# Performance work log

Hardware: AMD Instinct MI355X
Metric: run time of the kernel (lower is better)

Reference implementation:

```python
import jax, jax.numpy as jnp
import numpy as np

BATCH = 16384
N_MODES = 4096  # grid length == retained Fourier modes


def setup_inputs() -> dict:
    key = jax.random.key(0)
    k1, k2, k3 = jax.random.split(key, 3)
    inputs = jax.random.normal(k1, (BATCH, N_MODES), dtype=jnp.float32)
    # he_normal-style init for fourier weights, normal for linear weights
    fourier_weights = jax.random.normal(k2, (N_MODES,), dtype=jnp.float32) * np.sqrt(2.0 / N_MODES).astype(np.float32)
    linear_weights = jax.random.normal(k3, (N_MODES,), dtype=jnp.float32)
    return {"inputs": inputs, "fourier_weights": fourier_weights, "linear_weights": linear_weights}


def reference(inputs, fourier_weights, linear_weights):
    n_modes = fourier_weights.shape[0]
    # FFT along last axis (tf.signal.fft semantics), truncate to n_modes
    xf = jnp.fft.fft(inputs.astype(jnp.complex64), axis=-1)[:, :n_modes]
    # complex elementwise multiply by real weights cast to complex
    xf = xf * fourier_weights.astype(jnp.complex64)
    # inverse FFT over the truncated spectrum, take real part
    x = jnp.real(jnp.fft.ifft(xf, axis=-1)).astype(jnp.float32)
    # spectral branch scaled by linear weights + linear skip branch
    x = x * linear_weights
    z = inputs * linear_weights
    return jax.nn.relu(x + z)
```

## Files before the change

kernel.cpp:

```cpp
#include <hip/hip_runtime.h>
#include <math.h>

#define FFT_N   4096
#define THREADS 256
#define PADN    (FFT_N + (FFT_N >> 5))

__global__ void setup_g_kernel(const float* __restrict__ fw, float* __restrict__ gperm) {
    int p = blockIdx.x * blockDim.x + threadIdx.x;
    if (p >= FFT_N) return;
    unsigned k = ((p & 15u) << 8) | (p & 0xF0u) | ((unsigned)p >> 8);
    float wk  = fw[k];
    float wnk = fw[(FFT_N - k) & (FFT_N - 1)];
    gperm[p] = (0.5f * (wk + wnk) + 1.0f) * (1.0f / (float)FFT_N);
}

template<int DIR>
__device__ __forceinline__ void dft16(float xr[16], float xi[16]) {
    const float C1 = 0.9238795325112867f;
    const float S1 = 0.3826834323650898f;
    const float H  = 0.7071067811865476f;
    const float TCt[10] = {1.f, C1, H, S1, 0.f, -S1, -H, -C1, -1.f, -C1};
    const float TSt[10] = {0.f, S1, H, C1, 1.f,  C1, H,  S1,  0.f, -S1};
    float tr[16], ti[16];
    #pragma unroll
    for (int m0 = 0; m0 < 4; ++m0) {
        float ar = xr[m0+ 0], ai = xi[m0+ 0];
        float br = xr[m0+ 4], bi = xi[m0+ 4];
        float cr = xr[m0+ 8], ci = xi[m0+ 8];
        float dr = xr[m0+12], di = xi[m0+12];
        float t0r = ar+cr, t0i = ai+ci;
        float t1r = ar-cr, t1i = ai-ci;
        float t2r = br+dr, t2i = bi+di;
        float t3r = br-dr, t3i = bi-di;
        float A0r = t0r+t2r, A0i = t0i+t2i;
        float A2r = t0r-t2r, A2i = t0i-t2i;
        float A1r, A1i, A3r, A3i;
        if (DIR > 0) { A1r = t1r + t3i; A1i = t1i - t3r; A3r = t1r - t3i; A3i = t1i + t3r; }
        else         { A1r = t1r - t3i; A1i = t1i + t3r; A3r = t1r + t3i; A3i = t1i - t3r; }
        tr[0*4+m0] = A0r; ti[0*4+m0] = A0i;
        {
            float c = TCt[m0], s = (DIR > 0) ? -TSt[m0] : TSt[m0];
            float vr = A1r*c - A1i*s, vi = A1r*s + A1i*c;
            tr[1*4+m0] = vr; ti[1*4+m0] = vi;
        }
        {
            float c = TCt[2*m0], s = (DIR > 0) ? -TSt[2*m0] : TSt[2*m0];
            float vr = A2r*c - A2i*s, vi = A2r*s + A2i*c;
            tr[2*4+m0] = vr; ti[2*4+m0] = vi;
        }
        {
            float c = TCt[3*m0], s = (DIR > 0) ? -TSt[3*m0] : TSt[3*m0];
            float vr = A3r*c - A3i*s, vi = A3r*s + A3i*c;
            tr[3*4+m0] = vr; ti[3*4+m0] = vi;
        }
    }
    #pragma unroll
    for (int k0 = 0; k0 < 4; ++k0) {
        float ar = tr[k0*4+0], ai = ti[k0*4+0];
        float br = tr[k0*4+1], bi = ti[k0*4+1];
        float cr = tr[k0*4+2], ci = ti[k0*4+2];
        float dr = tr[k0*4+3], di = ti[k0*4+3];
        float t0r = ar+cr, t0i = ai+ci;
        float t1r = ar-cr, t1i = ai-ci;
        float t2r = br+dr, t2i = bi+di;
        float t3r = br-dr, t3i = bi-di;
        xr[k0+ 0] = t0r+t2r; xi[k0+ 0] = t0i+t2i;
        xr[k0+ 8] = t0r-t2r; xi[k0+ 8] = t0i-t2i;
        if (DIR > 0) {
            xr[k0+ 4] = t1r + t3i; xi[k0+ 4] = t1i - t3r;
            xr[k0+12] = t1r - t3i; xi[k0+12] = t1i + t3r;
        } else {
            xr[k0+ 4] = t1r - t3i; xi[k0+ 4] = t1i + t3r;
            xr[k0+12] = t1r + t3i; xi[k0+12] = t1i - t3r;
        }
    }
}

__device__ __forceinline__ void twiddle_apply(float xr[16], float xi[16], float ang1) {
    float s1, c1;
    __sincosf(ang1, &s1, &c1);
    float wc = c1, ws = s1;
    #pragma unroll
    for (int k = 1; k < 16; ++k) {
        float tv = xr[k];
        xr[k] = tv*wc - xi[k]*ws;
        xi[k] = tv*ws + xi[k]*wc;
        if (k < 15) { float nc = wc*c1 - ws*s1; ws = wc*s1 + ws*c1; wc = nc; }
    }
}

__global__ __launch_bounds__(THREADS, 4) void fourier_fft_kernel(
    const float* __restrict__ in, const float* __restrict__ gperm,
    const float* __restrict__ lw, float* __restrict__ out)
{
    __shared__ float re[PADN];
    __shared__ float im[PADN];
    const int t = threadIdx.x;
    const long long pair = blockIdx.x;
    const float* r0 = in + pair * (2LL * FFT_N);
    const float* r1 = r0 + FFT_N;

    const float CFA = -6.28318530717958647692f / 4096.0f;
    const float CFB = -6.28318530717958647692f / 256.0f;

    float xr[16], xi[16];

    #pragma unroll
    for (int k = 0; k < 16; ++k) {
        xr[k] = r0[t + 256*k];
        xi[k] = r1[t + 256*k];
    }

    dft16<1>(xr, xi);
    twiddle_apply(xr, xi, CFA * (float)t);
    #pragma unroll
    for (int k = 0; k < 16; ++k) { int s = t + 256*k; s += s>>5; re[s] = xr[k]; im[s] = xi[k]; }
    __syncthreads();

    const int jb = t & 15;
    const int baseB = (t >> 4)*256 + jb;
    #pragma unroll
    for (int k = 0; k < 16; ++k) { int s = baseB + 16*k; s += s>>5; xr[k] = re[s]; xi[k] = im[s]; }
    dft16<1>(xr, xi);
    twiddle_apply(xr, xi, CFB * (float)jb);
    #pragma unroll
    for (int k = 0; k < 16; ++k) { int s = baseB + 16*k; s += s>>5; re[s] = xr[k]; im[s] = xi[k]; }
    __syncthreads();

    #pragma unroll
    for (int k = 0; k < 16; ++k) { int s = 16*t + k; s += s>>5; xr[k] = re[s]; xi[k] = im[s]; }
    dft16<1>(xr, xi);
    {
        const float4* gp = (const float4*)(gperm + 16*t);
        #pragma unroll
        for (int q = 0; q < 4; ++q) {
            float4 g = gp[q];
            xr[4*q+0] *= g.x; xi[4*q+0] *= g.x;
            xr[4*q+1] *= g.y; xi[4*q+1] *= g.y;
            xr[4*q+2] *= g.z; xi[4*q+2] *= g.z;
            xr[4*q+3] *= g.w; xi[4*q+3] *= g.w;
        }
    }
    dft16<-1>(xr, xi);
    #pragma unroll
    for (int k = 0; k < 16; ++k) { int s = 16*t + k; s += s>>5; re[s] = xr[k]; im[s] = xi[k]; }
    __syncthreads();

    #pragma unroll
    for (int k = 0; k < 16; ++k) { int s = baseB + 16*k; s += s>>5; xr[k] = re[s]; xi[k] = im[s]; }
    twiddle_apply(xr, xi, -CFB * (float)jb);
    dft16<-1>(xr, xi);
    #pragma unroll
    for (int k = 0; k < 16; ++k) { int s = baseB + 16*k; s += s>>5; re[s] = xr[k]; im[s] = xi[k]; }
    __syncthreads();

    #pragma unroll
    for (int k = 0; k < 16; ++k) { int s = t + 256*k; s += s>>5; xr[k] = re[s]; xi[k] = im[s]; }
    twiddle_apply(xr, xi, -CFA * (float)t);
    dft16<-1>(xr, xi);

    float* o0 = out + pair * (2LL * FFT_N);
    #pragma unroll
    for (int k = 0; k < 16; ++k) {
        int i = t + 256*k;
        float l = lw[i];
        o0[i]         = fmaxf(xr[k]*l, 0.0f);
        o0[FFT_N + i] = fmaxf(xi[k]*l, 0.0f);
    }
}

extern "C" void kernel_launch(void* const* d_in, const int* in_sizes, int n_in,
                              void* d_out, int out_size, void* d_ws, size_t ws_size,
                              hipStream_t stream) {
    const float* inputs = (const float*)d_in[0];
    const float* fw     = (const float*)d_in[1];
    const float* lw     = (const float*)d_in[2];
    float* out   = (float*)d_out;
    float* gperm = (float*)d_ws;

    hipLaunchKernelGGL(setup_g_kernel, dim3(FFT_N / THREADS), dim3(THREADS), 0, stream,
                       fw, gperm);

    const int pairs = in_sizes[0] / (2 * FFT_N);
    hipLaunchKernelGGL(fourier_fft_kernel, dim3(pairs), dim3(THREADS), 0, stream,
                       inputs, gperm, lw, out);
}
```

Baseline: 119.8 us.

## Switch FFT from radix-16 three-pass to radix-8 four-pass with XOR-swizzled LDS

Rewrites the 4096-point forward/inverse FFT pair from three radix-16 passes with 256 threads into four radix-8 passes with 512 threads per block. This roughly halves per-thread register use so more waves can be resident, which should hide global and LDS latency better. Bank conflicts are now avoided with an XOR swizzle instead of padded shared arrays, and the gain-vector permutation is updated to the new digit-reversal order. In exchange there are more LDS round trips and barriers per row pair.

New measurement: 124.5 us. +4.0%, slower.

```diff
diff --git a/kernel.cpp b/kernel.cpp
--- a/kernel.cpp
+++ b/kernel.cpp
@@ -2,167 +2,165 @@
 #include <math.h>
 
 #define FFT_N   4096
-#define THREADS 256
-#define PADN    (FFT_N + (FFT_N >> 5))
+#define THREADS 512
+
+__device__ __forceinline__ int swz(int i) {
+    return i ^ ((i >> 5) & 31) ^ (((i >> 6) & 7) << 2);
+}
 
 __global__ void setup_g_kernel(const float* __restrict__ fw, float* __restrict__ gperm) {
     int p = blockIdx.x * blockDim.x + threadIdx.x;
     if (p >= FFT_N) return;
-    unsigned k = ((p & 15u) << 8) | (p & 0xF0u) | ((unsigned)p >> 8);
+    unsigned k = ((p & 7u) << 9) | (((p >> 3) & 7u) << 6) | (((p >> 6) & 7u) << 3) | ((p >> 9) & 7u);
     float wk  = fw[k];
     float wnk = fw[(FFT_N - k) & (FFT_N - 1)];
     gperm[p] = (0.5f * (wk + wnk) + 1.0f) * (1.0f / (float)FFT_N);
 }
 
 template<int DIR>
-__device__ __forceinline__ void dft16(float xr[16], float xi[16]) {
-    const float C1 = 0.9238795325112867f;
-    const float S1 = 0.3826834323650898f;
-    const float H  = 0.7071067811865476f;
-    const float TCt[10] = {1.f, C1, H, S1, 0.f, -S1, -H, -C1, -1.f, -C1};
-    const float TSt[10] = {0.f, S1, H, C1, 1.f,  C1, H,  S1,  0.f, -S1};
-    float tr[16], ti[16];
-    #pragma unroll
-    for (int m0 = 0; m0 < 4; ++m0) {
-        float ar = xr[m0+ 0], ai = xi[m0+ 0];
-        float br = xr[m0+ 4], bi = xi[m0+ 4];
-        float cr = xr[m0+ 8], ci = xi[m0+ 8];
-        float dr = xr[m0+12], di = xi[m0+12];
-        float t0r = ar+cr, t0i = ai+ci;
-        float t1r = ar-cr, t1i = ai-ci;
-        float t2r = br+dr, t2i = bi+di;
-        float t3r = br-dr, t3i = bi-di;
-        float A0r = t0r+t2r, A0i = t0i+t2i;
-        float A2r = t0r-t2r, A2i = t0i-t2i;
-        float A1r, A1i, A3r, A3i;
-        if (DIR > 0) { A1r = t1r + t3i; A1i = t1i - t3r; A3r = t1r - t3i; A3i = t1i + t3r; }
-        else         { A1r = t1r - t3i; A1i = t1i + t3r; A3r = t1r + t3i; A3i = t1i - t3r; }
-        tr[0*4+m0] = A0r; ti[0*4+m0] = A0i;
-        {
-            float c = TCt[m0], s = (DIR > 0) ? -TSt[m0] : TSt[m0];
-            float vr = A1r*c - A1i*s, vi = A1r*s + A1i*c;
-            tr[1*4+m0] = vr; ti[1*4+m0] = vi;
-        }
-        {
-            float c = TCt[2*m0], s = (DIR > 0) ? -TSt[2*m0] : TSt[2*m0];
-            float vr = A2r*c - A2i*s, vi = A2r*s + A2i*c;
-            tr[2*4+m0] = vr; ti[2*4+m0] = vi;
-        }
-        {
-            float c = TCt[3*m0], s = (DIR > 0) ? -TSt[3*m0] : TSt[3*m0];
-            float vr = A3r*c - A3i*s, vi = A3r*s + A3i*c;
-            tr[3*4+m0] = vr; ti[3*4+m0] = vi;
-        }
+__device__ __forceinline__ void dft8(float xr[8], float xi[8]) {
+    const float H = 0.7071067811865476f;
+    float u0r = xr[0]+xr[4], u0i = xi[0]+xi[4];
+    float u1r = xr[1]+xr[5], u1i = xi[1]+xi[5];
+    float u2r = xr[2]+xr[6], u2i = xi[2]+xi[6];
+    float u3r = xr[3]+xr[7], u3i = xi[3]+xi[7];
+    float v0r = xr[0]-xr[4], v0i = xi[0]-xi[4];
+    float v1r = xr[1]-xr[5], v1i = xi[1]-xi[5];
+    float v2r = xr[2]-xr[6], v2i = xi[2]-xi[6];
+    float v3r = xr[3]-xr[7], v3i = xi[3]-xi[7];
+    {
+        float r = v1r, m = v1i;
+        if (DIR > 0) { v1r = H*(r + m); v1i = H*(m - r); }
+        else         { v1r = H*(r - m); v1i = H*(m + r); }
     }
-    #pragma unroll
-    for (int k0 = 0; k0 < 4; ++k0) {
-        float ar = tr[k0*4+0], ai = ti[k0*4+0];
-        float br = tr[k0*4+1], bi = ti[k0*4+1];
-        float cr = tr[k0*4+2], ci = ti[k0*4+2];
-        float dr = tr[k0*4+3], di = ti[k0*4+3];
-        float t0r = ar+cr, t0i = ai+ci;
-        float t1r = ar-cr, t1i = ai-ci;
-        float t2r = br+dr, t2i = bi+di;
-        float t3r = br-dr, t3i = bi-di;
-        xr[k0+ 0] = t0r+t2r; xi[k0+ 0] = t0i+t2i;
-        xr[k0+ 8] = t0r-t2r; xi[k0+ 8] = t0i-t2i;
-        if (DIR > 0) {
-            xr[k0+ 4] = t1r + t3i; xi[k0+ 4] = t1i - t3r;
-            xr[k0+12] = t1r - t3i; xi[k0+12] = t1i + t3r;
-        } else {
-            xr[k0+ 4] = t1r - t3i; xi[k0+ 4] = t1i + t3r;
-            xr[k0+12] = t1r + t3i; xi[k0+12] = t1i - t3r;
-        }
+    {
+        float r = v2r, m = v2i;
+        if (DIR > 0) { v2r = m;  v2i = -r; }
+        else         { v2r = -m; v2i = r;  }
+    }
+    {
+        float r = v3r, m = v3i;
+        if (DIR > 0) { v3r = H*(m - r);  v3i = -H*(m + r); }
+        else         { v3r = -H*(m + r); v3i = H*(r - m);  }
+    }
+    {
+        float t0r=u0r+u2r, t0i=u0i+u2i, t1r=u0r-u2r, t1i=u0i-u2i;
+        float t2r=u1r+u3r, t2i=u1i+u3i, t3r=u1r-u3r, t3i=u1i-u3i;
+        xr[0]=t0r+t2r; xi[0]=t0i+t2i;
+        xr[4]=t0r-t2r; xi[4]=t0i-t2i;
+        if (DIR>0) { xr[2]=t1r+t3i; xi[2]=t1i-t3r; xr[6]=t1r-t3i; xi[6]=t1i+t3r; }
+        else       { xr[2]=t1r-t3i; xi[2]=t1i+t3r; xr[6]=t1r+t3i; xi[6]=t1i-t3r; }
+    }
+    {
+        float t0r=v0r+v2r, t0i=v0i+v2i, t1r=v0r-v2r, t1i=v0i-v2i;
+        float t2r=v1r+v3r, t2i=v1i+v3i, t3r=v1r-v3r, t3i=v1i-v3i;
+        xr[1]=t0r+t2r; xi[1]=t0i+t2i;
+        xr[5]=t0r-t2r; xi[5]=t0i-t2i;
+        if (DIR>0) { xr[3]=t1r+t3i; xi[3]=t1i-t3r; xr[7]=t1r-t3i; xi[7]=t1i+t3r; }
+        else       { xr[3]=t1r-t3i; xi[3]=t1i+t3r; xr[7]=t1r+t3i; xi[7]=t1i-t3r; }
     }
 }
 
-__device__ __forceinline__ void twiddle_apply(float xr[16], float xi[16], float ang1) {
-    float s1, c1;
-    __sincosf(ang1, &s1, &c1);
+__device__ __forceinline__ void twiddle8(float xr[8], float xi[8], float ang) {
+    float s1, c1; __sincosf(ang, &s1, &c1);
     float wc = c1, ws = s1;
     #pragma unroll
-    for (int k = 1; k < 16; ++k) {
+    for (int k = 1; k < 8; ++k) {
         float tv = xr[k];
         xr[k] = tv*wc - xi[k]*ws;
         xi[k] = tv*ws + xi[k]*wc;
-        if (k < 15) { float nc = wc*c1 - ws*s1; ws = wc*s1 + ws*c1; wc = nc; }
+        if (k < 7) { float nc = wc*c1 - ws*s1; ws = wc*s1 + ws*c1; wc = nc; }
     }
 }
 
-__global__ __launch_bounds__(THREADS, 4) void fourier_fft_kernel(
+__global__ __launch_bounds__(THREADS, 6) void fourier_fft_kernel(
     const float* __restrict__ in, const float* __restrict__ gperm,
     const float* __restrict__ lw, float* __restrict__ out)
 {
-    __shared__ float re[PADN];
-    __shared__ float im[PADN];
+    __shared__ float re[FFT_N];
+    __shared__ float im[FFT_N];
     const int t = threadIdx.x;
     const long long pair = blockIdx.x;
     const float* r0 = in + pair * (2LL * FFT_N);
     const float* r1 = r0 + FFT_N;
 
     const float CFA = -6.28318530717958647692f / 4096.0f;
-    const float CFB = -6.28318530717958647692f / 256.0f;
+    const float CFB = -6.28318530717958647692f / 512.0f;
+    const float CFC = -6.28318530717958647692f / 64.0f;
 
-    float xr[16], xi[16];
+    float xr[8], xi[8];
 
     #pragma unroll
-    for (int k = 0; k < 16; ++k) {
-        xr[k] = r0[t + 256*k];
-        xi[k] = r1[t + 256*k];
+    for (int k = 0; k < 8; ++k) {
+        xr[k] = r0[t + 512*k];
+        xi[k] = r1[t + 512*k];
     }
 
-    dft16<1>(xr, xi);
-    twiddle_apply(xr, xi, CFA * (float)t);
+    dft8<1>(xr, xi);
+    twiddle8(xr, xi, CFA * (float)t);
     #pragma unroll
-    for (int k = 0; k < 16; ++k) { int s = t + 256*k; s += s>>5; re[s] = xr[k]; im[s] = xi[k]; }
+    for (int k = 0; k < 8; ++k) { int s = swz(t + 512*k); re[s] = xr[k]; im[s] = xi[k]; }
     __syncthreads();
 
-    const int jb = t & 15;
-    const int baseB = (t >> 4)*256 + jb;
+    const int baseB = ((t >> 6) << 9) + (t & 63);
     #pragma unroll
-    for (int k = 0; k < 16; ++k) { int s = baseB + 16*k; s += s>>5; xr[k] = re[s]; xi[k] = im[s]; }
-    dft16<1>(xr, xi);
-    twiddle_apply(xr, xi, CFB * (float)jb);
+    for (int k = 0; k < 8; ++k) { int s = swz(baseB + 64*k); xr[k] = re[s]; xi[k] = im[s]; }
+    dft8<1>(xr, xi);
+    twiddle8(xr, xi, CFB * (float)(t & 63));
     #pragma unroll
-    for (int k = 0; k < 16; ++k) { int s = baseB + 16*k; s += s>>5; re[s] = xr[k]; im[s] = xi[k]; }
+    for (int k = 0; k < 8; ++k) { int s = swz(baseB + 64*k); re[s] = xr[k]; im[s] = xi[k]; }
+    __syncthreads();
+
+    const int baseC = ((t >> 3) << 6) + (t & 7);
+    #pragma unroll
+    for (int k = 0; k < 8; ++k) { int s = swz(baseC + 8*k); xr[k] = re[s]; xi[k] = im[s]; }
+    dft8<1>(xr, xi);
+    twiddle8(xr, xi, CFC * (float)(t & 7));
+    #pragma unroll
+    for (int k = 0; k < 8; ++k) { int s = swz(baseC + 8*k); re[s] = xr[k]; im[s] = xi[k]; }
     __syncthreads();
 
     #pragma unroll
-    for (int k = 0; k < 16; ++k) { int s = 16*t + k; s += s>>5; xr[k] = re[s]; xi[k] = im[s]; }
-    dft16<1>(xr, xi);
+    for (int k = 0; k < 8; ++k) { int s = swz(8*t + k); xr[k] = re[s]; xi[k] = im[s]; }
+    dft8<1>(xr, xi);
     {
-        const float4* gp = (const float4*)(gperm + 16*t);
-        #pragma unroll
-        for (int q = 0; q < 4; ++q) {
-            float4 g = gp[q];
-            xr[4*q+0] *= g.x; xi[4*q+0] *= g.x;
-            xr[4*q+1] *= g.y; xi[4*q+1] *= g.y;
-            xr[4*q+2] *= g.z; xi[4*q+2] *= g.z;
-            xr[4*q+3] *= g.w; xi[4*q+3] *= g.w;
-        }
+        const float4* gp = (const float4*)(gperm + 8*t);
+        float4 g0 = gp[0], g1 = gp[1];
+        xr[0] *= g0.x; xi[0] *= g0.x;  xr[1] *= g0.y; xi[1] *= g0.y;
+        xr[2] *= g0.z; xi[2] *= g0.z;  xr[3] *= g0.w; xi[3] *= g0.w;
+        xr[4] *= g1.x; xi[4] *= g1.x;  xr[5] *= g1.y; xi[5] *= g1.y;
+        xr[6] *= g1.z; xi[6] *= g1.z;  xr[7] *= g1.w; xi[7] *= g1.w;
     }
-    dft16<-1>(xr, xi);
+    dft8<-1>(xr, xi);
     #pragma unroll
-    for (int k = 0; k < 16; ++k) { int s = 16*t + k; s += s>>5; re[s] = xr[k]; im[s] = xi[k]; }
+    for (int k = 0; k < 8; ++k) { int s = swz(8*t + k); re[s] = xr[k]; im[s] = xi[k]; }
     __syncthreads();
 
     #pragma unroll
-    for (int k = 0; k < 16; ++k) { int s = baseB + 16*k; s += s>>5; xr[k] = re[s]; xi[k] = im[s]; }
-    twiddle_apply(xr, xi, -CFB * (float)jb);
-    dft16<-1>(xr, xi);
+    for (int k = 0; k < 8; ++k) { int s = swz(baseC + 8*k); xr[k] = re[s]; xi[k] = im[s]; }
+    twiddle8(xr, xi, -CFC * (float)(t & 7));
+    dft8<-1>(xr, xi);
     #pragma unroll
-    for (int k = 0; k < 16; ++k) { int s = baseB + 16*k; s += s>>5; re[s] = xr[k]; im[s] = xi[k]; }
+    for (int k = 0; k < 8; ++k) { int s = swz(baseC + 8*k); re[s] = xr[k]; im[s] = xi[k]; }
     __syncthreads();
 
     #pragma unroll
-    for (int k = 0; k < 16; ++k) { int s = t + 256*k; s += s>>5; xr[k] = re[s]; xi[k] = im[s]; }
-    twiddle_apply(xr, xi, -CFA * (float)t);
-    dft16<-1>(xr, xi);
+    for (int k = 0; k < 8; ++k) { int s = swz(baseB + 64*k); xr[k] = re[s]; xi[k] = im[s]; }
+    twiddle8(xr, xi, -CFB * (float)(t & 63));
+    dft8<-1>(xr, xi);
+    #pragma unroll
+    for (int k = 0; k < 8; ++k) { int s = swz(baseB + 64*k); re[s] = xr[k]; im[s] = xi[k]; }
+    __syncthreads();
+
+    #pragma unroll
+    for (int k = 0; k < 8; ++k) { int s = swz(t + 512*k); xr[k] = re[s]; xi[k] = im[s]; }
+    twiddle8(xr, xi, -CFA * (float)t);
+    dft8<-1>(xr, xi);
 
     float* o0 = out + pair * (2LL * FFT_N);
     #pragma unroll
-    for (int k = 0; k < 16; ++k) {
-        int i = t + 256*k;
+    for (int k = 0; k < 8; ++k) {
+        int i = t + 512*k;
         float l = lw[i];
         o0[i]         = fmaxf(xr[k]*l, 0.0f);
         o0[FFT_N + i] = fmaxf(xi[k]*l, 0.0f);
@@ -178,7 +176,7 @@
     float* out   = (float*)d_out;
     float* gperm = (float*)d_ws;
 
-    hipLaunchKernelGGL(setup_g_kernel, dim3(FFT_N / THREADS), dim3(THREADS), 0, stream,
+    hipLaunchKernelGGL(setup_g_kernel, dim3(FFT_N / 256), dim3(256), 0, stream,
                        fw, gperm);
 
     const int pairs = in_sizes[0] / (2 * FFT_N);
```
